# Kernel optimization log

Measured on AMD Instinct MI355X. Metric: run time of the kernel, lower is better.

The kernel has to match this reference:

```python
import jax, jax.numpy as jnp
import numpy as np

B, D, E, K = 8192, 4096, 64, 2

def setup_inputs() -> dict:
    key = jax.random.key(0)
    k1, k2 = jax.random.split(key)
    x = jax.random.normal(k1, (B, D), dtype=jnp.float32)
    gate_w = jax.random.normal(k2, (E, D), dtype=jnp.float32) * (1.0 / np.sqrt(D))
    temperature = jnp.ones((), dtype=jnp.float32)
    return {"x": x, "gate_w": gate_w, "temperature": temperature}

def reference(x, gate_w, temperature):
    # logits = (x @ W^T) / temperature  -> [B, E]
    logits = jnp.einsum('bd,ed->be', x, gate_w) / temperature
    top_logits, top_idx = jax.lax.top_k(logits, K)          # [B, K]
    routing_weights = jax.nn.softmax(top_logits, axis=-1)    # [B, K]
    rows = jnp.arange(x.shape[0])[:, None]                   # [B, 1]
    routing_matrix = jnp.zeros((x.shape[0], E), dtype=x.dtype).at[rows, top_idx].set(routing_weights)
    return routing_matrix, top_idx
```

## Files before the change

kernel.cpp:

```cpp
#include <hip/hip_runtime.h>
#include <stdint.h>
#include <stddef.h>


typedef __attribute__((ext_vector_type(8))) short short8;
typedef __attribute__((ext_vector_type(4))) float f32x4;

static constexpr int kB = 8192;
static constexpr int kD = 4096;
static constexpr int kE = 64;
static constexpr int kSteps = kD / 32;
static constexpr int kWv = 8;
static constexpr int kRows = 16;
static constexpr int kBK = 256;
static constexpr int kBufs = kD / kBK;
static constexpr int kRowPad = 260;

__device__ __forceinline__ uint32_t bf16_rne(float v) {
    uint32_t u = __builtin_bit_cast(uint32_t, v);
    return (u + 0x7FFFu + ((u >> 16) & 1u)) >> 16;
}

__device__ __forceinline__ void cvt8(const f32x4& a0, const f32x4& a1,
                                     short8& ah, short8& al) {
#pragma unroll
    for (int j = 0; j < 4; ++j) {
        float xv = a0[j];
        uint32_t u  = __builtin_bit_cast(uint32_t, xv);
        uint32_t rh = (u + 0x7FFFu + ((u >> 16) & 1u)) & 0xFFFF0000u;
        ah[j] = (short)(rh >> 16);
        al[j] = (short)bf16_rne(xv - __builtin_bit_cast(float, rh));
        float yv = a1[j];
        uint32_t u2  = __builtin_bit_cast(uint32_t, yv);
        uint32_t rh2 = (u2 + 0x7FFFu + ((u2 >> 16) & 1u)) & 0xFFFF0000u;
        ah[j + 4] = (short)(rh2 >> 16);
        al[j + 4] = (short)bf16_rne(yv - __builtin_bit_cast(float, rh2));
    }
}

__device__ __forceinline__ void glds16(const float* g, float* l) {
    __builtin_amdgcn_global_load_lds(
        (const __attribute__((address_space(1))) unsigned int*)g,
        (__attribute__((address_space(3))) unsigned int*)l, 16, 0, 0);
}

__global__ __launch_bounds__(256) void prep_w_kernel(
    const float* __restrict__ w, short* __restrict__ w_hi, short* __restrict__ w_lo)
{
    int tid  = blockIdx.x * 256 + threadIdx.x;
    int lane = tid & 63;
    int s    = (tid >> 6) & (kSteps - 1);
    int nt   = tid >> 13;
    int e = nt * 16 + (lane & 15);
    int k = s * 32 + (lane >> 4) * 8;
    const float* src = w + (size_t)e * kD + k;
    short8 hi, lo;
#pragma unroll
    for (int j = 0; j < 8; ++j) {
        float xv = src[j];
        uint32_t u  = __builtin_bit_cast(uint32_t, xv);
        uint32_t rh = (u + 0x7FFFu + ((u >> 16) & 1u)) & 0xFFFF0000u;
        hi[j] = (short)(rh >> 16);
        float lf = xv - __builtin_bit_cast(float, rh);
        lo[j] = (short)bf16_rne(lf);
    }
    ((short8*)w_hi)[tid] = hi;
    ((short8*)w_lo)[tid] = lo;
}

__global__ __launch_bounds__(512, 4) void router_kernel(
    const float* __restrict__ x, const short8* __restrict__ w_hi,
    const short8* __restrict__ w_lo, const float* __restrict__ temp,
    float* __restrict__ out_mat, float* __restrict__ out_idx)
{
    const int lane = threadIdx.x & 63;
    const int wv   = threadIdx.x >> 6;
    const int quad = lane >> 4;
    const int mr   = lane & 15;
    const int row0 = blockIdx.x * kRows;

    __shared__ __align__(16) float smem[2 * kRows * kRowPad];
    float (*lds_x)[kRows][kRowPad] = (float (*)[kRows][kRowPad])smem;
    float (*part)[kRows][kE]       = (float (*)[kRows][kE])smem;

    f32x4 acc[4];
#pragma unroll
    for (int nt = 0; nt < 4; ++nt) acc[nt] = (f32x4){0.f, 0.f, 0.f, 0.f};

    short8 wbh[2][4], wbl[2][4];

#pragma unroll
    for (int seg = 0; seg < 2; ++seg) {
        const int r = 2 * wv + seg;
        glds16(x + (size_t)(row0 + r) * kD + lane * 4, &lds_x[0][r][0]);
    }
#pragma unroll
    for (int nt = 0; nt < 4; ++nt) {
        wbh[0][nt] = w_hi[(size_t)(nt * kSteps + wv) * 64 + lane];
        wbl[0][nt] = w_lo[(size_t)(nt * kSteps + wv) * 64 + lane];
    }

#pragma unroll 2
    for (int b = 0; b < kBufs; ++b) {
        const int pb = b & 1;
        __syncthreads();

        if (b + 1 < kBufs) {
#pragma unroll
            for (int seg = 0; seg < 2; ++seg) {
                const int r = 2 * wv + seg;
                glds16(x + (size_t)(row0 + r) * kD + (b + 1) * kBK + lane * 4,
                       &lds_x[pb ^ 1][r][0]);
            }
            const int s = (b + 1) * kWv + wv;
#pragma unroll
            for (int nt = 0; nt < 4; ++nt) {
                wbh[pb ^ 1][nt] = w_hi[(size_t)(nt * kSteps + s) * 64 + lane];
                wbl[pb ^ 1][nt] = w_lo[(size_t)(nt * kSteps + s) * 64 + lane];
            }
        }

        const float* ap = &lds_x[pb][mr][wv * 32 + quad * 8];
        f32x4 a0 = *(const f32x4*)ap;
        f32x4 a1 = *(const f32x4*)(ap + 4);
        short8 ah, al;
        cvt8(a0, a1, ah, al);
#pragma unroll
        for (int nt = 0; nt < 4; ++nt) {
            acc[nt] = __builtin_amdgcn_mfma_f32_16x16x32_bf16(al, wbl[pb][nt], acc[nt], 0, 0, 0);
            acc[nt] = __builtin_amdgcn_mfma_f32_16x16x32_bf16(al, wbh[pb][nt], acc[nt], 0, 0, 0);
            acc[nt] = __builtin_amdgcn_mfma_f32_16x16x32_bf16(ah, wbl[pb][nt], acc[nt], 0, 0, 0);
            acc[nt] = __builtin_amdgcn_mfma_f32_16x16x32_bf16(ah, wbh[pb][nt], acc[nt], 0, 0, 0);
        }
    }

    __syncthreads();

#pragma unroll
    for (int nt = 0; nt < 4; ++nt)
#pragma unroll
        for (int r = 0; r < 4; ++r)
            part[wv][quad * 4 + r][nt * 16 + mr] = acc[nt][r];
    __syncthreads();

    const float invT = 1.0f / temp[0];
#pragma unroll
    for (int p = 0; p < 2; ++p) {
        const int row = wv + p * kWv;
        float v = 0.f;
#pragma unroll
        for (int s = 0; s < kWv; ++s)
            v += part[s][row][lane];

        float v1 = v; int i1 = lane;
#pragma unroll
        for (int m = 1; m < 64; m <<= 1) {
            float ov = __shfl_xor(v1, m, 64);
            int   oi = __shfl_xor(i1, m, 64);
            if (ov > v1 || (ov == v1 && oi < i1)) { v1 = ov; i1 = oi; }
        }
        float vm = (lane == i1) ? -3.0e38f : v;
        float v2 = vm; int i2 = lane;
#pragma unroll
        for (int m = 1; m < 64; m <<= 1) {
            float ov = __shfl_xor(v2, m, 64);
            int   oi = __shfl_xor(i2, m, 64);
            if (ov > v2 || (ov == v2 && oi < i2)) { v2 = ov; i2 = oi; }
        }

        float e  = expf((v2 - v1) * invT);
        float sm = 1.0f + e;
        out_mat[(size_t)(row0 + row) * kE + lane] =
            (lane == i1) ? (1.0f / sm) : ((lane == i2) ? (e / sm) : 0.0f);
        if (lane == 0)
            ((float2*)out_idx)[row0 + row] = make_float2((float)i1, (float)i2);
    }
}

extern "C" void kernel_launch(void* const* d_in, const int* in_sizes, int n_in,
                              void* d_out, int out_size, void* d_ws, size_t ws_size,
                              hipStream_t stream) {
    const float* x    = (const float*)d_in[0];
    const float* gw   = (const float*)d_in[1];
    const float* temp = (const float*)d_in[2];

    float* out_mat = (float*)d_out;
    float* out_idx = (float*)d_out + (size_t)kB * kE;

    short* w_hi = (short*)d_ws;
    short* w_lo = w_hi + (size_t)kE * kD;

    prep_w_kernel<<<128, 256, 0, stream>>>(gw, w_hi, w_lo);

    router_kernel<<<kB / kRows, 512, 0, stream>>>(
        x, (const short8*)w_hi, (const short8*)w_lo, temp, out_mat, out_idx);
}
```

Baseline: 203.7 us.

## Process 32 rows per block, reuse W fragments, and XOR-swizzle LDS layout

Doubles the rows handled per workgroup from 16 to 32, so each loaded hi/lo weight fragment feeds two row-tiles of MFMAs. This halves global weight traffic per row and the number of blocks. The padded LDS rows are replaced by an XOR swizzle on the global-to-LDS copy and on the reads, to avoid bank conflicts without padding. The cost is more accumulator registers and LDS per block, so occupancy drops (launch bounds go from 4 to 2) and the grid shrinks to 256 blocks.

```diff
diff --git a/kernel.cpp b/kernel.cpp
--- a/kernel.cpp
+++ b/kernel.cpp
@@ -11,10 +11,10 @@
 static constexpr int kE = 64;
 static constexpr int kSteps = kD / 32;
 static constexpr int kWv = 8;
-static constexpr int kRows = 16;
+static constexpr int kRows = 32;
 static constexpr int kBK = 256;
 static constexpr int kBufs = kD / kBK;
-static constexpr int kRowPad = 260;
+static constexpr int kRowF = 256;
 
 __device__ __forceinline__ uint32_t bf16_rne(float v) {
     uint32_t u = __builtin_bit_cast(uint32_t, v);
@@ -68,7 +68,7 @@
     ((short8*)w_lo)[tid] = lo;
 }
 
-__global__ __launch_bounds__(512, 4) void router_kernel(
+__global__ __launch_bounds__(512, 2) void router_kernel(
     const float* __restrict__ x, const short8* __restrict__ w_hi,
     const short8* __restrict__ w_lo, const float* __restrict__ temp,
     float* __restrict__ out_mat, float* __restrict__ out_idx)
@@ -79,20 +79,23 @@
     const int mr   = lane & 15;
     const int row0 = blockIdx.x * kRows;
 
-    __shared__ __align__(16) float smem[2 * kRows * kRowPad];
-    float (*lds_x)[kRows][kRowPad] = (float (*)[kRows][kRowPad])smem;
-    float (*part)[kRows][kE]       = (float (*)[kRows][kE])smem;
-
-    f32x4 acc[4];
-#pragma unroll
-    for (int nt = 0; nt < 4; ++nt) acc[nt] = (f32x4){0.f, 0.f, 0.f, 0.f};
+    __shared__ __align__(16) float smem[2 * kRows * kRowF];
+    float (*part)[kRows][kE] = (float (*)[kRows][kE])smem;
+
+    f32x4 acc0[4], acc1[4];
+#pragma unroll
+    for (int nt = 0; nt < 4; ++nt) {
+        acc0[nt] = (f32x4){0.f, 0.f, 0.f, 0.f};
+        acc1[nt] = (f32x4){0.f, 0.f, 0.f, 0.f};
+    }
 
     short8 wbh[2][4], wbl[2][4];
 
 #pragma unroll
-    for (int seg = 0; seg < 2; ++seg) {
-        const int r = 2 * wv + seg;
-        glds16(x + (size_t)(row0 + r) * kD + lane * 4, &lds_x[0][r][0]);
+    for (int seg = 0; seg < 4; ++seg) {
+        const int r = 4 * wv + seg;
+        glds16(x + (size_t)(row0 + r) * kD + ((lane * 4) ^ ((r & 7) << 2)),
+               &smem[r * kRowF]);
     }
 #pragma unroll
     for (int nt = 0; nt < 4; ++nt) {
@@ -107,10 +110,11 @@
 
         if (b + 1 < kBufs) {
 #pragma unroll
-            for (int seg = 0; seg < 2; ++seg) {
-                const int r = 2 * wv + seg;
-                glds16(x + (size_t)(row0 + r) * kD + (b + 1) * kBK + lane * 4,
-                       &lds_x[pb ^ 1][r][0]);
+            for (int seg = 0; seg < 4; ++seg) {
+                const int r = 4 * wv + seg;
+                glds16(x + (size_t)(row0 + r) * kD + (b + 1) * kBK
+                         + ((lane * 4) ^ ((r & 7) << 2)),
+                       &smem[(pb ^ 1) * kRows * kRowF + r * kRowF]);
             }
             const int s = (b + 1) * kWv + wv;
 #pragma unroll
@@ -120,17 +124,26 @@
             }
         }
 
-        const float* ap = &lds_x[pb][mr][wv * 32 + quad * 8];
-        f32x4 a0 = *(const f32x4*)ap;
-        f32x4 a1 = *(const f32x4*)(ap + 4);
-        short8 ah, al;
-        cvt8(a0, a1, ah, al);
+        const int ss = (mr & 7) << 2;
+        const int c0 = wv * 32 + quad * 8;
+        const float* bb = &smem[pb * kRows * kRowF];
+        f32x4 a0 = *(const f32x4*)&bb[(size_t)mr * kRowF + ((c0) ^ ss)];
+        f32x4 a1 = *(const f32x4*)&bb[(size_t)mr * kRowF + ((c0 + 4) ^ ss)];
+        f32x4 b0 = *(const f32x4*)&bb[(size_t)(mr + 16) * kRowF + ((c0) ^ ss)];
+        f32x4 b1 = *(const f32x4*)&bb[(size_t)(mr + 16) * kRowF + ((c0 + 4) ^ ss)];
+        short8 ah0, al0, ah1, al1;
+        cvt8(a0, a1, ah0, al0);
+        cvt8(b0, b1, ah1, al1);
 #pragma unroll
         for (int nt = 0; nt < 4; ++nt) {
-            acc[nt] = __builtin_amdgcn_mfma_f32_16x16x32_bf16(al, wbl[pb][nt], acc[nt], 0, 0, 0);
-            acc[nt] = __builtin_amdgcn_mfma_f32_16x16x32_bf16(al, wbh[pb][nt], acc[nt], 0, 0, 0);
-            acc[nt] = __builtin_amdgcn_mfma_f32_16x16x32_bf16(ah, wbl[pb][nt], acc[nt], 0, 0, 0);
-            acc[nt] = __builtin_amdgcn_mfma_f32_16x16x32_bf16(ah, wbh[pb][nt], acc[nt], 0, 0, 0);
+            acc0[nt] = __builtin_amdgcn_mfma_f32_16x16x32_bf16(al0, wbl[pb][nt], acc0[nt], 0, 0, 0);
+            acc0[nt] = __builtin_amdgcn_mfma_f32_16x16x32_bf16(al0, wbh[pb][nt], acc0[nt], 0, 0, 0);
+            acc0[nt] = __builtin_amdgcn_mfma_f32_16x16x32_bf16(ah0, wbl[pb][nt], acc0[nt], 0, 0, 0);
+            acc0[nt] = __builtin_amdgcn_mfma_f32_16x16x32_bf16(ah0, wbh[pb][nt], acc0[nt], 0, 0, 0);
+            acc1[nt] = __builtin_amdgcn_mfma_f32_16x16x32_bf16(al1, wbl[pb][nt], acc1[nt], 0, 0, 0);
+            acc1[nt] = __builtin_amdgcn_mfma_f32_16x16x32_bf16(al1, wbh[pb][nt], acc1[nt], 0, 0, 0);
+            acc1[nt] = __builtin_amdgcn_mfma_f32_16x16x32_bf16(ah1, wbl[pb][nt], acc1[nt], 0, 0, 0);
+            acc1[nt] = __builtin_amdgcn_mfma_f32_16x16x32_bf16(ah1, wbh[pb][nt], acc1[nt], 0, 0, 0);
         }
     }
 
@@ -139,13 +152,15 @@
 #pragma unroll
     for (int nt = 0; nt < 4; ++nt)
 #pragma unroll
-        for (int r = 0; r < 4; ++r)
-            part[wv][quad * 4 + r][nt * 16 + mr] = acc[nt][r];
+        for (int r = 0; r < 4; ++r) {
+            part[wv][quad * 4 + r][nt * 16 + mr]      = acc0[nt][r];
+            part[wv][16 + quad * 4 + r][nt * 16 + mr] = acc1[nt][r];
+        }
     __syncthreads();
 
     const float invT = 1.0f / temp[0];
 #pragma unroll
-    for (int p = 0; p < 2; ++p) {
+    for (int p = 0; p < 4; ++p) {
         const int row = wv + p * kWv;
         float v = 0.f;
 #pragma unroll
```

Result: no change. 202.6 us (-0.5%).
